# Kernel tuning notes

Hardware: AMD Instinct MI355X
Metric: run time of the kernel (lower is better)

## Reference

```python
import jax, jax.numpy as jnp
import numpy as np

B, D, H1, H2, E, O = 32768, 256, 512, 256, 16, 64


def setup_inputs() -> dict:
    key = jax.random.key(0)
    ks = jax.random.split(key, 12)
    s = lambda fan_in: 1.0 / np.sqrt(fan_in)
    return {
        "x": jax.random.normal(ks[0], (B, D), dtype=jnp.float32),
        "gate_w": jax.random.normal(ks[1], (D, E), dtype=jnp.float32) * s(D),
        "gate_b": jnp.zeros((E,), dtype=jnp.float32),
        "W1": jax.random.normal(ks[2], (E, D, H1), dtype=jnp.float32) * s(D),
        "b1": jnp.zeros((E, H1), dtype=jnp.float32),
        "W2": jax.random.normal(ks[3], (E, H1, H2), dtype=jnp.float32) * s(H1),
        "b2": jnp.zeros((E, H2), dtype=jnp.float32),
        "W3": jax.random.normal(ks[4], (E, H2, O), dtype=jnp.float32) * s(H2),
        "b3": jnp.zeros((E, O), dtype=jnp.float32),
        "head_w": jax.random.normal(ks[5], (O, 1), dtype=jnp.float32) * s(O),
        "head_b": jnp.zeros((1,), dtype=jnp.float32),
    }


def reference(x, gate_w, gate_b, W1, b1, W2, b2, W3, b3, head_w, head_b):
    # gating: softmax over experts, [B, E]
    gates = jax.nn.softmax(x @ gate_w + gate_b, axis=-1)
    # all-expert dense MLP as batched GEMMs over leading expert axis
    h1 = jax.nn.relu(jnp.einsum('bd,edh->ebh', x, W1) + b1[:, None, :])   # [E,B,H1]
    h2 = jax.nn.relu(jnp.einsum('ebh,ehk->ebk', h1, W2) + b2[:, None, :])  # [E,B,H2]
    eo = jnp.einsum('ebk,eko->ebo', h2, W3) + b3[:, None, :]               # [E,B,O]
    # gated combination: sum_e gates[b,e] * eo[e,b,:]
    fused = jnp.einsum('be,ebo->bo', gates, eo)                            # [B,O]
    yts = (fused @ head_w + head_b)[:, 0]                                  # [B]
    return yts
```

## Files before the change

### kernel.cpp

```cpp
#include <hip/hip_runtime.h>

#define B_TOK 32768
#define D_IN  256
#define H1D   512
#define H2D   256
#define NE    16
#define NO    64

typedef _Float16 half8 __attribute__((ext_vector_type(8)));
typedef _Float16 half4 __attribute__((ext_vector_type(4)));
typedef float   float4_t __attribute__((ext_vector_type(4)));

__global__ void prep_kernel(const float* __restrict__ W1, const float* __restrict__ W2,
                            const float* __restrict__ W3, const float* __restrict__ b3,
                            const float* __restrict__ hw, const float* __restrict__ gw,
                            _Float16* __restrict__ w1p, _Float16* __restrict__ w2p,
                            float* __restrict__ w3h, float* __restrict__ c3,
                            _Float16* __restrict__ gwp) {
  int blk = blockIdx.x;
  int tid = threadIdx.x;
  if (blk < 1024) {
    int t = blk * 256 + tid;
    int lane = t & 63;
    int kt   = (t >> 6) & 7;
    int ntg  = (t >> 9) & 31;
    int e    = t >> 14;
    int n  = ntg * 16 + (lane & 15);
    int kb = kt * 32 + (lane >> 4) * 8;
    half8 v;
    #pragma unroll
    for (int j = 0; j < 8; ++j)
      v[j] = (_Float16)W1[((size_t)(e * D_IN + kb + j)) * H1D + n];
    *(half8*)(w1p + (size_t)t * 8) = v;
  } else if (blk < 2048) {
    int t = (blk - 1024) * 256 + tid;
    int lane = t & 63;
    int ktg  = (t >> 6) & 15;
    int ntg  = (t >> 10) & 15;
    int e    = t >> 14;
    int n  = ntg * 16 + (lane & 15);
    int kb = ktg * 32 + (lane >> 4) * 8;
    half8 v;
    #pragma unroll
    for (int j = 0; j < 8; ++j)
      v[j] = (_Float16)W2[((size_t)(e * H1D + kb + j)) * H2D + n];
    *(half8*)(w2p + (size_t)t * 8) = v;
  } else if (blk < 2065) {
    int t = (blk - 2048) * 256 + tid;
    if (t < NE * H2D) {
      int e = t >> 8, h = t & 255;
      float s = 0.f;
      #pragma unroll
      for (int o = 0; o < NO; ++o) s = fmaf(W3[((size_t)(e * H2D + h)) * NO + o], hw[o], s);
      w3h[t] = s;
    } else if (t < NE * H2D + NE) {
      int e = t - NE * H2D;
      float s = 0.f;
      #pragma unroll
      for (int o = 0; o < NO; ++o) s = fmaf(b3[e * NO + o], hw[o], s);
      c3[e] = s;
    }
  } else {
    for (int t = tid; t < 512; t += 256) {
      int lane = t & 63;
      int kt   = t >> 6;
      int e  = lane & 15;
      int kb = kt * 32 + (lane >> 4) * 8;
      half8 v;
      #pragma unroll
      for (int j = 0; j < 8; ++j)
        v[j] = (_Float16)gw[(kb + j) * NE + e];
      *(half8*)(gwp + (size_t)t * 8) = v;
    }
  }
}

#define H1STR 520

__global__ __launch_bounds__(256, 2) void moe_main(
    const float* __restrict__ x,
    const float* __restrict__ b1,
    const float* __restrict__ b2,
    const _Float16* __restrict__ w1p,
    const _Float16* __restrict__ w2p,
    const _Float16* __restrict__ gwp,
    const float* __restrict__ gb,
    const float* __restrict__ w3h,
    const float* __restrict__ c3,
    const float* __restrict__ head_b,
    float* __restrict__ out) {
  __shared__ _Float16 h1_lds[64 * H1STR];
  __shared__ float g_lds[64 * 17];
  __shared__ float fin[4 * 64];

  const int tid  = threadIdx.x;
  const int w    = tid >> 6;
  const int lane = tid & 63;
  const int q    = lane >> 4;
  const int l16  = lane & 15;
  const int m0   = blockIdx.x * 64;

  half8 xf[4][8];
  #pragma unroll
  for (int nt = 0; nt < 4; ++nt) {
    const float* xr = x + (size_t)(m0 + nt * 16 + l16) * D_IN + q * 8;
    #pragma unroll
    for (int kt = 0; kt < 8; ++kt) {
      float4_t v0 = *(const float4_t*)(xr + kt * 32);
      float4_t v1 = *(const float4_t*)(xr + kt * 32 + 4);
      half8 h;
      h[0] = (_Float16)v0[0]; h[1] = (_Float16)v0[1];
      h[2] = (_Float16)v0[2]; h[3] = (_Float16)v0[3];
      h[4] = (_Float16)v1[0]; h[5] = (_Float16)v1[1];
      h[6] = (_Float16)v1[2]; h[7] = (_Float16)v1[3];
      xf[nt][kt] = h;
    }
  }

  {
    float gbv = gb[l16];
    #pragma unroll
    for (int mt = 0; mt < 4; ++mt) {
      if (mt == w) {
        float4_t lg = (float4_t){0.f, 0.f, 0.f, 0.f};
        #pragma unroll
        for (int kt = 0; kt < 8; ++kt) {
          half8 bfr = *(const half8*)(gwp + (size_t)kt * 512 + lane * 8);
          lg = __builtin_amdgcn_mfma_f32_16x16x32_f16(xf[mt][kt], bfr, lg, 0, 0, 0);
        }
        #pragma unroll
        for (int r = 0; r < 4; ++r) {
          float v = lg[r] + gbv;
          float m = v;
          m = fmaxf(m, __shfl_xor(m, 1));
          m = fmaxf(m, __shfl_xor(m, 2));
          m = fmaxf(m, __shfl_xor(m, 4));
          m = fmaxf(m, __shfl_xor(m, 8));
          float p = __expf(v - m);
          float s = p;
          s += __shfl_xor(s, 1);
          s += __shfl_xor(s, 2);
          s += __shfl_xor(s, 4);
          s += __shfl_xor(s, 8);
          g_lds[(mt * 16 + q * 4 + r) * 17 + l16] = p / s;
        }
      }
    }
  }

  float yacc[4][4];
  #pragma unroll
  for (int mt = 0; mt < 4; ++mt)
    #pragma unroll
    for (int r = 0; r < 4; ++r) yacc[mt][r] = 0.f;

  for (int e = 0; e < NE; ++e) {
    #pragma unroll
    for (int ch = 0; ch < 2; ++ch) {
      float4_t a1[4][4];
      #pragma unroll
      for (int mt = 0; mt < 4; ++mt)
        #pragma unroll
        for (int nt = 0; nt < 4; ++nt)
          a1[mt][nt] = (float4_t){0.f, 0.f, 0.f, 0.f};

      const _Float16* wbase =
          w1p + ((size_t)((e * 32 + ch * 16 + w * 4) * 8)) * 512 + lane * 8;
      #pragma unroll
      for (int kt = 0; kt < 8; ++kt) {
        half8 wc[4];
        #pragma unroll
        for (int mt = 0; mt < 4; ++mt)
          wc[mt] = *(const half8*)(wbase + (size_t)(mt * 8 + kt) * 512);
        #pragma unroll
        for (int mt = 0; mt < 4; ++mt)
          #pragma unroll
          for (int nt = 0; nt < 4; ++nt)
            a1[mt][nt] = __builtin_amdgcn_mfma_f32_16x16x32_f16(
                wc[mt], xf[nt][kt], a1[mt][nt], 0, 0, 0);
      }

      #pragma unroll
      for (int mt = 0; mt < 4; ++mt) {
        int colbase = ch * 256 + (w * 4 + mt) * 16 + q * 4;
        float4_t bb = *(const float4_t*)(b1 + e * H1D + colbase);
        #pragma unroll
        for (int nt = 0; nt < 4; ++nt) {
          half4 hv;
          #pragma unroll
          for (int r = 0; r < 4; ++r)
            hv[r] = (_Float16)fmaxf(a1[mt][nt][r] + bb[r], 0.f);
          *(half4*)(h1_lds + (nt * 16 + l16) * H1STR + colbase) = hv;
        }
      }
    }

    float b2v[4], w3v[4];
    #pragma unroll
    for (int nt = 0; nt < 4; ++nt) {
      int n = w * 64 + nt * 16 + l16;
      b2v[nt] = b2[e * H2D + n];
      w3v[nt] = w3h[e * H2D + n];
    }

    __syncthreads();

    float4_t h2[4][4];
    #pragma unroll
    for (int mt = 0; mt < 4; ++mt)
      #pragma unroll
      for (int nt = 0; nt < 4; ++nt)
        h2[mt][nt] = (float4_t){0.f, 0.f, 0.f, 0.f};

    const _Float16* w2base =
        w2p + ((size_t)((e * 16 + w * 4) * 16)) * 512 + lane * 8;
    #pragma unroll
    for (int kt = 0; kt < 16; ++kt) {
      half8 w2c[4];
      #pragma unroll
      for (int nt = 0; nt < 4; ++nt)
        w2c[nt] = *(const half8*)(w2base + (size_t)(nt * 16 + kt) * 512);
      half8 hac[4];
      #pragma unroll
      for (int mt = 0; mt < 4; ++mt)
        hac[mt] = *(const half8*)(h1_lds + (mt * 16 + l16) * H1STR + kt * 32 + q * 8);
      #pragma unroll
      for (int mt = 0; mt < 4; ++mt)
        #pragma unroll
        for (int nt = 0; nt < 4; ++nt)
          h2[mt][nt] = __builtin_amdgcn_mfma_f32_16x16x32_f16(
              hac[mt], w2c[nt], h2[mt][nt], 0, 0, 0);
    }

    #pragma unroll
    for (int mt = 0; mt < 4; ++mt) {
      #pragma unroll
      for (int r = 0; r < 4; ++r) {
        float s = 0.f;
        #pragma unroll
        for (int nt = 0; nt < 4; ++nt)
          s += fmaxf(h2[mt][nt][r] + b2v[nt], 0.f) * w3v[nt];
        yacc[mt][r] += g_lds[(mt * 16 + q * 4 + r) * 17 + e] * s;
      }
    }
    __syncthreads();
  }

  #pragma unroll
  for (int mt = 0; mt < 4; ++mt) {
    #pragma unroll
    for (int r = 0; r < 4; ++r) {
      float v = yacc[mt][r];
      v += __shfl_xor(v, 1);
      v += __shfl_xor(v, 2);
      v += __shfl_xor(v, 4);
      v += __shfl_xor(v, 8);
      yacc[mt][r] = v;
    }
  }
  if (l16 == 0) {
    #pragma unroll
    for (int mt = 0; mt < 4; ++mt)
      #pragma unroll
      for (int r = 0; r < 4; ++r)
        fin[w * 64 + mt * 16 + q * 4 + r] = yacc[mt][r];
  }
  __syncthreads();
  if (tid < 64) {
    float sum = fin[tid] + fin[64 + tid] + fin[128 + tid] + fin[192 + tid];
    float gc = 0.f;
    #pragma unroll
    for (int e = 0; e < NE; ++e) gc += g_lds[tid * 17 + e] * c3[e];
    out[m0 + tid] = sum + gc + head_b[0];
  }
}

extern "C" void kernel_launch(void* const* d_in, const int* in_sizes, int n_in,
                              void* d_out, int out_size, void* d_ws, size_t ws_size,
                              hipStream_t stream) {
  const float* x      = (const float*)d_in[0];
  const float* gate_w = (const float*)d_in[1];
  const float* gate_b = (const float*)d_in[2];
  const float* W1     = (const float*)d_in[3];
  const float* b1     = (const float*)d_in[4];
  const float* W2     = (const float*)d_in[5];
  const float* b2     = (const float*)d_in[6];
  const float* W3     = (const float*)d_in[7];
  const float* b3     = (const float*)d_in[8];
  const float* head_w = (const float*)d_in[9];
  const float* head_b = (const float*)d_in[10];
  float* out = (float*)d_out;

  char* ws = (char*)d_ws;
  _Float16* w1p = (_Float16*)(ws);
  _Float16* w2p = (_Float16*)(ws + 4194304);
  _Float16* gwp = (_Float16*)(ws + 8388608);
  float*    w3h = (float*)(ws + 8396800);
  float*    c3  = (float*)(ws + 8413184);

  hipLaunchKernelGGL(prep_kernel, dim3(2066), dim3(256), 0, stream,
                     W1, W2, W3, b3, head_w, gate_w, w1p, w2p, w3h, c3, gwp);
  hipLaunchKernelGGL(moe_main, dim3(B_TOK / 64), dim3(256), 0, stream,
                     x, b1, b2, w1p, w2p, gwp, gate_b, w3h, c3, head_b, out);
}
```

Before: 410.9 us.

## Stage x tile in LDS and interleave H1 chunks with layer-2 accumulation

The x tile is no longer held as 32 half8 registers per lane. It is converted once to fp16 in LDS and reread from there for the gating GEMM and for every layer-1 GEMM. Layer 2 now consumes each 256-column half of h1 right after it is produced, so the h1 buffer shrinks to half width and h2 accumulates across the two chunks. This cuts register pressure and trims the h1 part of shared memory while adding an x region, aiming at better occupancy or fewer spills. The cost is extra LDS reads and more barriers per expert.

```diff
diff --git a/kernel.cpp b/kernel.cpp
--- a/kernel.cpp
+++ b/kernel.cpp
@@ -75,7 +75,7 @@
   }
 }
 
-#define H1STR 520
+#define H1CSTR 266
 
 __global__ __launch_bounds__(256, 2) void moe_main(
     const float* __restrict__ x,
@@ -89,7 +89,8 @@
     const float* __restrict__ c3,
     const float* __restrict__ head_b,
     float* __restrict__ out) {
-  __shared__ _Float16 h1_lds[64 * H1STR];
+  __shared__ _Float16 x_lds[32 * 512];
+  __shared__ _Float16 h1c[64 * H1CSTR];
   __shared__ float g_lds[64 * 17];
   __shared__ float fin[4 * 64];
 
@@ -100,51 +101,44 @@
   const int l16  = lane & 15;
   const int m0   = blockIdx.x * 64;
 
-  half8 xf[4][8];
   #pragma unroll
-  for (int nt = 0; nt < 4; ++nt) {
-    const float* xr = x + (size_t)(m0 + nt * 16 + l16) * D_IN + q * 8;
-    #pragma unroll
-    for (int kt = 0; kt < 8; ++kt) {
-      float4_t v0 = *(const float4_t*)(xr + kt * 32);
-      float4_t v1 = *(const float4_t*)(xr + kt * 32 + 4);
-      half8 h;
-      h[0] = (_Float16)v0[0]; h[1] = (_Float16)v0[1];
-      h[2] = (_Float16)v0[2]; h[3] = (_Float16)v0[3];
-      h[4] = (_Float16)v1[0]; h[5] = (_Float16)v1[1];
-      h[6] = (_Float16)v1[2]; h[7] = (_Float16)v1[3];
-      xf[nt][kt] = h;
-    }
-  }
+  for (int f = 0; f < 8; ++f) {
+    const float* xr = x + (size_t)(m0 + w * 16 + l16) * D_IN + f * 32 + q * 8;
+    float4_t v0 = *(const float4_t*)(xr);
+    float4_t v1 = *(const float4_t*)(xr + 4);
+    half8 h;
+    h[0] = (_Float16)v0[0]; h[1] = (_Float16)v0[1];
+    h[2] = (_Float16)v0[2]; h[3] = (_Float16)v0[3];
+    h[4] = (_Float16)v1[0]; h[5] = (_Float16)v1[1];
+    h[6] = (_Float16)v1[2]; h[7] = (_Float16)v1[3];
+    *(half8*)(x_lds + (size_t)(w * 8 + f) * 512 + lane * 8) = h;
+  }
+  __syncthreads();
 
   {
     float gbv = gb[l16];
-    #pragma unroll
-    for (int mt = 0; mt < 4; ++mt) {
-      if (mt == w) {
-        float4_t lg = (float4_t){0.f, 0.f, 0.f, 0.f};
-        #pragma unroll
-        for (int kt = 0; kt < 8; ++kt) {
-          half8 bfr = *(const half8*)(gwp + (size_t)kt * 512 + lane * 8);
-          lg = __builtin_amdgcn_mfma_f32_16x16x32_f16(xf[mt][kt], bfr, lg, 0, 0, 0);
-        }
-        #pragma unroll
-        for (int r = 0; r < 4; ++r) {
-          float v = lg[r] + gbv;
-          float m = v;
-          m = fmaxf(m, __shfl_xor(m, 1));
-          m = fmaxf(m, __shfl_xor(m, 2));
-          m = fmaxf(m, __shfl_xor(m, 4));
-          m = fmaxf(m, __shfl_xor(m, 8));
-          float p = __expf(v - m);
-          float s = p;
-          s += __shfl_xor(s, 1);
-          s += __shfl_xor(s, 2);
-          s += __shfl_xor(s, 4);
-          s += __shfl_xor(s, 8);
-          g_lds[(mt * 16 + q * 4 + r) * 17 + l16] = p / s;
-        }
-      }
+    float4_t lg = (float4_t){0.f, 0.f, 0.f, 0.f};
+    #pragma unroll
+    for (int kt = 0; kt < 8; ++kt) {
+      half8 xa = *(const half8*)(x_lds + (size_t)(w * 8 + kt) * 512 + lane * 8);
+      half8 bfr = *(const half8*)(gwp + (size_t)kt * 512 + lane * 8);
+      lg = __builtin_amdgcn_mfma_f32_16x16x32_f16(xa, bfr, lg, 0, 0, 0);
+    }
+    #pragma unroll
+    for (int r = 0; r < 4; ++r) {
+      float v = lg[r] + gbv;
+      float m = v;
+      m = fmaxf(m, __shfl_xor(m, 1));
+      m = fmaxf(m, __shfl_xor(m, 2));
+      m = fmaxf(m, __shfl_xor(m, 4));
+      m = fmaxf(m, __shfl_xor(m, 8));
+      float p = __expf(v - m);
+      float s = p;
+      s += __shfl_xor(s, 1);
+      s += __shfl_xor(s, 2);
+      s += __shfl_xor(s, 4);
+      s += __shfl_xor(s, 8);
+      g_lds[(w * 16 + q * 4 + r) * 17 + l16] = p / s;
     }
   }
 
@@ -155,6 +149,13 @@
     for (int r = 0; r < 4; ++r) yacc[mt][r] = 0.f;
 
   for (int e = 0; e < NE; ++e) {
+    float4_t h2[4][4];
+    #pragma unroll
+    for (int mt = 0; mt < 4; ++mt)
+      #pragma unroll
+      for (int nt = 0; nt < 4; ++nt)
+        h2[mt][nt] = (float4_t){0.f, 0.f, 0.f, 0.f};
+
     #pragma unroll
     for (int ch = 0; ch < 2; ++ch) {
       float4_t a1[4][4];
@@ -164,35 +165,63 @@
         for (int nt = 0; nt < 4; ++nt)
           a1[mt][nt] = (float4_t){0.f, 0.f, 0.f, 0.f};
 
-      const _Float16* wbase =
+      const _Float16* w1e =
           w1p + ((size_t)((e * 32 + ch * 16 + w * 4) * 8)) * 512 + lane * 8;
       #pragma unroll
       for (int kt = 0; kt < 8; ++kt) {
         half8 wc[4];
         #pragma unroll
         for (int mt = 0; mt < 4; ++mt)
-          wc[mt] = *(const half8*)(wbase + (size_t)(mt * 8 + kt) * 512);
+          wc[mt] = *(const half8*)(w1e + (size_t)(mt * 8 + kt) * 512);
+        half8 xb[4];
+        #pragma unroll
+        for (int nt = 0; nt < 4; ++nt)
+          xb[nt] = *(const half8*)(x_lds + (size_t)(nt * 8 + kt) * 512 + lane * 8);
         #pragma unroll
         for (int mt = 0; mt < 4; ++mt)
           #pragma unroll
           for (int nt = 0; nt < 4; ++nt)
             a1[mt][nt] = __builtin_amdgcn_mfma_f32_16x16x32_f16(
-                wc[mt], xf[nt][kt], a1[mt][nt], 0, 0, 0);
+                wc[mt], xb[nt], a1[mt][nt], 0, 0, 0);
       }
 
       #pragma unroll
       for (int mt = 0; mt < 4; ++mt) {
-        int colbase = ch * 256 + (w * 4 + mt) * 16 + q * 4;
-        float4_t bb = *(const float4_t*)(b1 + e * H1D + colbase);
+        int colbase = (w * 4 + mt) * 16 + q * 4;
+        float4_t bb = *(const float4_t*)(b1 + e * H1D + ch * 256 + colbase);
         #pragma unroll
         for (int nt = 0; nt < 4; ++nt) {
           half4 hv;
           #pragma unroll
           for (int r = 0; r < 4; ++r)
             hv[r] = (_Float16)fmaxf(a1[mt][nt][r] + bb[r], 0.f);
-          *(half4*)(h1_lds + (nt * 16 + l16) * H1STR + colbase) = hv;
+          *(half4*)(h1c + (nt * 16 + l16) * H1CSTR + colbase) = hv;
         }
       }
+
+      __syncthreads();
+
+      const _Float16* w2e =
+          w2p + ((size_t)((e * 16 + w * 4) * 16 + ch * 8)) * 512 + lane * 8;
+      #pragma unroll
+      for (int kt = 0; kt < 8; ++kt) {
+        half8 w2c[4];
+        #pragma unroll
+        for (int nt = 0; nt < 4; ++nt)
+          w2c[nt] = *(const half8*)(w2e + (size_t)(nt * 16 + kt) * 512);
+        half8 hac[4];
+        #pragma unroll
+        for (int mt = 0; mt < 4; ++mt)
+          hac[mt] = *(const half8*)(h1c + (mt * 16 + l16) * H1CSTR + kt * 32 + q * 8);
+        #pragma unroll
+        for (int mt = 0; mt < 4; ++mt)
+          #pragma unroll
+          for (int nt = 0; nt < 4; ++nt)
+            h2[mt][nt] = __builtin_amdgcn_mfma_f32_16x16x32_f16(
+                hac[mt], w2c[nt], h2[mt][nt], 0, 0, 0);
+      }
+
+      __syncthreads();
     }
 
     float b2v[4], w3v[4];
@@ -202,36 +231,6 @@
       b2v[nt] = b2[e * H2D + n];
       w3v[nt] = w3h[e * H2D + n];
     }
-
-    __syncthreads();
-
-    float4_t h2[4][4];
-    #pragma unroll
-    for (int mt = 0; mt < 4; ++mt)
-      #pragma unroll
-      for (int nt = 0; nt < 4; ++nt)
-        h2[mt][nt] = (float4_t){0.f, 0.f, 0.f, 0.f};
-
-    const _Float16* w2base =
-        w2p + ((size_t)((e * 16 + w * 4) * 16)) * 512 + lane * 8;
-    #pragma unroll
-    for (int kt = 0; kt < 16; ++kt) {
-      half8 w2c[4];
-      #pragma unroll
-      for (int nt = 0; nt < 4; ++nt)
-        w2c[nt] = *(const half8*)(w2base + (size_t)(nt * 16 + kt) * 512);
-      half8 hac[4];
-      #pragma unroll
-      for (int mt = 0; mt < 4; ++mt)
-        hac[mt] = *(const half8*)(h1_lds + (mt * 16 + l16) * H1STR + kt * 32 + q * 8);
-      #pragma unroll
-      for (int mt = 0; mt < 4; ++mt)
-        #pragma unroll
-        for (int nt = 0; nt < 4; ++nt)
-          h2[mt][nt] = __builtin_amdgcn_mfma_f32_16x16x32_f16(
-              hac[mt], w2c[nt], h2[mt][nt], 0, 0, 0);
-    }
-
     #pragma unroll
     for (int mt = 0; mt < 4; ++mt) {
       #pragma unroll
@@ -243,7 +242,6 @@
         yacc[mt][r] += g_lds[(mt * 16 + q * 4 + r) * 17 + e] * s;
       }
     }
-    __syncthreads();
   }
 
   #pragma unroll
```

After: 363.9 us. 1.13x faster.
